# Performance work log

Measured on AMD Instinct MI355X. Metric: run time of the kernel, lower is better.

The kernel has to match this reference:

```python
import jax, jax.numpy as jnp
import numpy as np

N_HEADS = 16


def setup_inputs() -> dict:
    key = jax.random.key(0)
    ks = jax.random.split(key, 5)
    B, S, D = 2, 2048, 1024
    scale = 1.0 / np.sqrt(D)
    return {
        "x": jax.random.normal(ks[0], (B, S, D), dtype=jnp.float32),
        "w_in": jax.random.normal(ks[1], (3 * D, D), dtype=jnp.float32) * scale,
        "b_in": jax.random.normal(ks[2], (3 * D,), dtype=jnp.float32) * 0.01,
        "w_out": jax.random.normal(ks[3], (D, D), dtype=jnp.float32) * scale,
        "b_out": jax.random.normal(ks[4], (D,), dtype=jnp.float32) * 0.01,
        "mask": 1,
    }


def reference(x, w_in, b_in, w_out, b_out, mask):
    b, s, d = x.shape
    h = N_HEADS
    dh = d // h
    # fused QKV projection (torch Linear: x @ W^T + b)
    qkv = jnp.einsum("bsd,ed->bse", x, w_in) + b_in  # [b, s, 3d]
    q, k, v = jnp.split(qkv, 3, axis=-1)
    # [b, s, d] -> [b, h, s, dh]
    q = q.reshape(b, s, h, dh).transpose(0, 2, 1, 3)
    k = k.reshape(b, s, h, dh).transpose(0, 2, 1, 3)
    v = v.reshape(b, s, h, dh).transpose(0, 2, 1, 3)
    att = jnp.einsum("bhqd,bhkd->bhqk", q, k)
    if mask:
        causal = jnp.triu(jnp.ones((s, s), dtype=bool), k=1)
        att = jnp.where(causal, -jnp.inf, att)
    att = att / jnp.sqrt(jnp.asarray(dh, att.dtype))
    att = jax.nn.softmax(att, axis=-1)
    out = jnp.einsum("bhqk,bhkd->bhqd", att, v)  # [b, h, s, dh]
    out = out.transpose(0, 2, 1, 3).reshape(b, s, d)
    return jnp.einsum("bsd,ed->bse", out, w_out) + b_out
```

## Files before the change

kernel.cpp:

```cpp
#include <hip/hip_runtime.h>
#include <hip/hip_bf16.h>
#include <cmath>

typedef __hip_bfloat16 bf16;
typedef short v8s __attribute__((ext_vector_type(8)));
typedef short v4s __attribute__((ext_vector_type(4)));
typedef float v4f __attribute__((ext_vector_type(4)));

#define AS1(p) ((__attribute__((address_space(1))) void*)(p))
#define AS3(p) ((__attribute__((address_space(3))) void*)(p))

__device__ __forceinline__ v4f mfma_bf16(v8s a, v8s b, v4f c) {
    return __builtin_amdgcn_mfma_f32_16x16x32_bf16(a, b, c, 0, 0, 0);
}

__device__ __forceinline__ short bf16_bits(float f) {
    return __builtin_bit_cast(short, __float2bfloat16(f));
}

__global__ __launch_bounds__(256)
void cvt_all(const float* __restrict__ x, const float* __restrict__ w_in,
             const float* __restrict__ w_out, bf16* __restrict__ xb,
             bf16* __restrict__ wib, bf16* __restrict__ wob)
{
    const int i = blockIdx.x * 256 + threadIdx.x;
    const float* src; bf16* dst; int j;
    if (i < 1048576)      { src = x;     dst = xb;  j = i; }
    else if (i < 1835008) { src = w_in;  dst = wib; j = i - 1048576; }
    else                  { src = w_out; dst = wob; j = i - 1835008; }
    const float4 v = ((const float4*)src)[j];
    v4s p;
    p.x = bf16_bits(v.x); p.y = bf16_bits(v.y);
    p.z = bf16_bits(v.z); p.w = bf16_bits(v.w);
    ((v4s*)dst)[j] = p;
}

template<int NF>
__global__ __launch_bounds__(256)
void gemm_bt(const bf16* __restrict__ A, const bf16* __restrict__ Bt,
             const float* __restrict__ bias, bf16* __restrict__ C,
             float* __restrict__ Cf, int N, int K, int lda)
{
    constexpr int BN = NF * 32;
    __shared__ __align__(16) bf16 As[128 * 64];
    __shared__ __align__(16) bf16 Bs[BN * 64];

    const int t    = threadIdx.x;
    const int lane = t & 63;
    const int wave = t >> 6;
    const int l16  = lane & 15;
    const int quad = lane >> 4;
    const int m0   = blockIdx.y * 128;
    const int n0   = blockIdx.x * BN;
    const int wm   = (wave >> 1) * 64;
    const int wn   = (wave & 1) * (NF * 16);

    const v4f zf = {0.f, 0.f, 0.f, 0.f};
    v4f acc[4][NF];
#pragma unroll
    for (int i = 0; i < 4; ++i)
#pragma unroll
        for (int j = 0; j < NF; ++j) acc[i][j] = zf;

    const int sr  = t >> 3;
    const int swz = ((t & 7) ^ (sr & 7)) * 8;
    const bf16* gA = A  + (size_t)(m0 + sr) * lda + swz;
    const bf16* gB = Bt + (size_t)(n0 + sr) * K + swz;
    char* lA = (char*)As + t * 16;
    char* lB = (char*)Bs + t * 16;

    for (int k0 = 0; k0 < K; k0 += 64) {
#pragma unroll
        for (int i = 0; i < 4; ++i)
            __builtin_amdgcn_global_load_lds(AS1(gA + (size_t)(i * 32) * lda + k0),
                                             AS3(lA + i * 4096), 16, 0, 0);
#pragma unroll
        for (int i = 0; i < NF; ++i)
            __builtin_amdgcn_global_load_lds(AS1(gB + (size_t)(i * 32) * K + k0),
                                             AS3(lB + i * 4096), 16, 0, 0);
        __syncthreads();

        v8s af[4][2], bfr[NF][2];
#pragma unroll
        for (int mi = 0; mi < 4; ++mi)
#pragma unroll
            for (int ks = 0; ks < 2; ++ks)
                af[mi][ks] = *(const v8s*)(As + (wm + mi * 16 + l16) * 64
                                           + (((ks * 4 + quad) ^ (l16 & 7)) * 8));
#pragma unroll
        for (int ni = 0; ni < NF; ++ni)
#pragma unroll
            for (int ks = 0; ks < 2; ++ks)
                bfr[ni][ks] = *(const v8s*)(Bs + (wn + ni * 16 + l16) * 64
                                            + (((ks * 4 + quad) ^ (l16 & 7)) * 8));
#pragma unroll
        for (int ks = 0; ks < 2; ++ks)
#pragma unroll
            for (int mi = 0; mi < 4; ++mi)
#pragma unroll
                for (int ni = 0; ni < NF; ++ni)
                    acc[mi][ni] = mfma_bf16(af[mi][ks], bfr[ni][ks], acc[mi][ni]);
        __syncthreads();
    }

#pragma unroll
    for (int ni = 0; ni < NF; ++ni) {
        const int col = n0 + wn + ni * 16 + l16;
        const float bv = bias[col];
#pragma unroll
        for (int mi = 0; mi < 4; ++mi) {
#pragma unroll
            for (int r = 0; r < 4; ++r) {
                const int row = m0 + wm + mi * 16 + quad * 4 + r;
                const float fv = acc[mi][ni][r] + bv;
                if (Cf) Cf[(size_t)row * N + col] = fv;
                else    C [(size_t)row * N + col] = __float2bfloat16(fv);
            }
        }
    }
}

__global__ __launch_bounds__(256)
void vtrans(const bf16* __restrict__ qkv, bf16* __restrict__ Vt)
{
    __shared__ short Ts[64][72];
    const int t  = threadIdx.x;
    const int st = blockIdx.x;
    const int bh = blockIdx.y;
    const int b = bh >> 4, h = bh & 15;
    const int s0 = st * 64;
    {
        const int i = t >> 2, j0 = (t & 3) * 16;
        const bf16* src = qkv + (size_t)(b * 2048 + s0 + i) * 3072 + 2048 + h * 64 + j0;
        const v8s a0 = *(const v8s*)(src);
        const v8s a1 = *(const v8s*)(src + 8);
        *(v8s*)&Ts[i][j0]     = a0;
        *(v8s*)&Ts[i][j0 + 8] = a1;
    }
    __syncthreads();
    {
        const int d = t >> 2, seg = (t & 3) * 16;
        v8s o0, o1;
#pragma unroll
        for (int m = 0; m < 8; ++m) { o0[m] = Ts[seg + m][d]; o1[m] = Ts[seg + 8 + m][d]; }
        bf16* dst = Vt + (size_t)(bh * 64 + d) * 2048 + s0 + seg;
        *(v8s*)dst       = o0;
        *(v8s*)(dst + 8) = o1;
    }
}

#define M_STATIC 14.0f
__global__ __launch_bounds__(256)
void attn(bf16* __restrict__ qkv, const bf16* __restrict__ Vt)
{
    __shared__ __align__(16) bf16 Ks[2][64 * 64];
    __shared__ __align__(16) bf16 Vs[2][64 * 64];
    __shared__ __align__(16) short Ps[4][16 * 72];

    const int t    = threadIdx.x;
    const int lane = t & 63;
    const int w    = t >> 6;
    const int l16  = lane & 15;
    const int quad = lane >> 4;
    const int id   = blockIdx.x;
    const int bh   = id & 31;
    const int qb   = 31 - (id >> 5);
    const int b = bh >> 4, h = bh & 15;
    const int T = qb + 1;
    const int rowq = qb * 64 + w * 16;

    v8s qf[2];
    {
        const bf16* Qb = qkv + (size_t)(b * 2048 + rowq + l16) * 3072 + h * 64 + quad * 8;
        qf[0] = *(const v8s*)(Qb);
        qf[1] = *(const v8s*)(Qb + 32);
    }

    const int sr  = t >> 3;
    const int swz = ((t & 7) ^ (sr & 7)) * 8;
    const bf16* kbase = qkv + (size_t)(b * 2048 + sr) * 3072 + 1024 + h * 64 + swz;
    const bf16* vbase = Vt + (size_t)(bh * 64 + sr) * 2048 + swz;
    char* kd = (char*)&Ks[0][0] + t * 16;
    char* vd = (char*)&Vs[0][0] + t * 16;

    __builtin_amdgcn_global_load_lds(AS1(kbase),                     AS3(kd),        16, 0, 0);
    __builtin_amdgcn_global_load_lds(AS1(kbase + (size_t)32 * 3072), AS3(kd + 4096), 16, 0, 0);
    __builtin_amdgcn_global_load_lds(AS1(vbase),                     AS3(vd),        16, 0, 0);
    __builtin_amdgcn_global_load_lds(AS1(vbase + (size_t)32 * 2048), AS3(vd + 4096), 16, 0, 0);

    const v4f zf = {0.f, 0.f, 0.f, 0.f};
    v4f o[4] = {zf, zf, zf, zf};
    float lsum[4] = {0.f, 0.f, 0.f, 0.f};
    short* Pw = &Ps[w][0];
    const int xsw = (l16 & 7) * 8;

    for (int tile = 0; tile < T; ++tile) {
        const int buf = tile & 1;
        __syncthreads();
        if (tile + 1 < T) {
            const int nb = buf ^ 1;
            const bf16* ksrc = kbase + (size_t)((tile + 1) * 64) * 3072;
            const bf16* vsrc = vbase + (tile + 1) * 64;
            char* kdn = (char*)&Ks[nb][0] + t * 16;
            char* vdn = (char*)&Vs[nb][0] + t * 16;
            __builtin_amdgcn_global_load_lds(AS1(ksrc),                     AS3(kdn),        16, 0, 0);
            __builtin_amdgcn_global_load_lds(AS1(ksrc + (size_t)32 * 3072), AS3(kdn + 4096), 16, 0, 0);
            __builtin_amdgcn_global_load_lds(AS1(vsrc),                     AS3(vdn),        16, 0, 0);
            __builtin_amdgcn_global_load_lds(AS1(vsrc + (size_t)32 * 2048), AS3(vdn + 4096), 16, 0, 0);
        }

        v4f s[4] = {zf, zf, zf, zf};
#pragma unroll
        for (int ks = 0; ks < 2; ++ks)
#pragma unroll
            for (int ct = 0; ct < 4; ++ct) {
                const v8s kf = *(const v8s*)(&Ks[buf][0] + (ct * 16 + l16) * 64
                                             + (((ks * 4 + quad) * 8) ^ xsw));
                s[ct] = mfma_bf16(qf[ks], kf, s[ct]);
            }

        if (tile == T - 1) {
            const int colb = tile * 64;
            const int rowb = rowq + quad * 4;
#pragma unroll
            for (int ct = 0; ct < 4; ++ct) {
                const int col = colb + ct * 16 + l16;
#pragma unroll
                for (int r = 0; r < 4; ++r) {
                    const float p = (col > rowb + r)
                        ? 0.f : __expf(fmaf(s[ct][r], 0.125f, -M_STATIC));
                    lsum[r] += p;
                    Pw[(quad * 4 + r) * 72 + ct * 16 + l16] = bf16_bits(p);
                }
            }
        } else {
#pragma unroll
            for (int ct = 0; ct < 4; ++ct)
#pragma unroll
                for (int r = 0; r < 4; ++r) {
                    const float p = __expf(fmaf(s[ct][r], 0.125f, -M_STATIC));
                    lsum[r] += p;
                    Pw[(quad * 4 + r) * 72 + ct * 16 + l16] = bf16_bits(p);
                }
        }
        asm volatile("s_waitcnt lgkmcnt(0)" ::: "memory");

#pragma unroll
        for (int ks = 0; ks < 2; ++ks) {
            const v8s pf = *(const v8s*)(Pw + l16 * 72 + ks * 32 + quad * 8);
#pragma unroll
            for (int nt = 0; nt < 4; ++nt) {
                const v8s vf = *(const v8s*)(&Vs[buf][0] + (nt * 16 + l16) * 64
                                             + (((ks * 4 + quad) * 8) ^ xsw));
                o[nt] = mfma_bf16(pf, vf, o[nt]);
            }
        }
    }

#pragma unroll
    for (int r = 0; r < 4; ++r) {
        float l = lsum[r];
        l += __shfl_xor(l, 1); l += __shfl_xor(l, 2);
        l += __shfl_xor(l, 4); l += __shfl_xor(l, 8);
        lsum[r] = fmaxf(l, 1e-30f);
    }

#pragma unroll
    for (int nt = 0; nt < 4; ++nt)
#pragma unroll
        for (int r = 0; r < 4; ++r) {
            const int row = rowq + quad * 4 + r;
            qkv[(size_t)(b * 2048 + row) * 3072 + 2048 + h * 64 + nt * 16 + l16] =
                __float2bfloat16(o[nt][r] / lsum[r]);
        }
}

extern "C" void kernel_launch(void* const* d_in, const int* in_sizes, int n_in,
                              void* d_out, int out_size, void* d_ws, size_t ws_size,
                              hipStream_t stream)
{
    (void)in_sizes; (void)n_in; (void)out_size; (void)ws_size;
    const float* x     = (const float*)d_in[0];
    const float* w_in  = (const float*)d_in[1];
    const float* b_in  = (const float*)d_in[2];
    const float* w_out = (const float*)d_in[3];
    const float* b_out = (const float*)d_in[4];
    float* out = (float*)d_out;

    bf16* ws     = (bf16*)d_ws;
    bf16* xb     = ws;
    bf16* w_inb  = xb     + (size_t)4096 * 1024;
    bf16* w_outb = w_inb  + (size_t)3072 * 1024;
    bf16* qkv    = w_outb + (size_t)1024 * 1024;
    bf16* vt     = (bf16*)d_out;

    cvt_all<<<8192, 256, 0, stream>>>(x, w_in, w_out, xb, w_inb, w_outb);

    gemm_bt<4><<<dim3(24, 32), dim3(256), 0, stream>>>(xb, w_inb, b_in, qkv, nullptr,
                                                       3072, 1024, 1024);
    vtrans<<<dim3(32, 32), dim3(256), 0, stream>>>(qkv, vt);
    attn<<<1024, 256, 0, stream>>>(qkv, vt);
    gemm_bt<2><<<dim3(16, 32), dim3(256), 0, stream>>>(qkv + 2048, w_outb, b_out, nullptr,
                                                       out, 1024, 1024, 3072);
}
```

Baseline: 194.2 us.

## Double-buffer GEMM LDS tiles with K-step 32 and prefetch next tile

Reworks the bf16 GEMM main loop to use two LDS buffers of half depth (K tile 32 instead of 64). The next tile's async global-to-LDS loads are issued right after the barrier so they overlap the current tile's MFMA work, and one of the two barriers per iteration is dropped. The swizzle is rewritten for the 32-wide rows. Each iteration now does half the MFMA work, so there is more barrier overhead per unit of compute. The B-tile staging also assumes NF is 2 or 4.

```diff
diff --git a/kernel.cpp b/kernel.cpp
--- a/kernel.cpp
+++ b/kernel.cpp
@@ -42,8 +42,8 @@
              float* __restrict__ Cf, int N, int K, int lda)
 {
     constexpr int BN = NF * 32;
-    __shared__ __align__(16) bf16 As[128 * 64];
-    __shared__ __align__(16) bf16 Bs[BN * 64];
+    __shared__ __align__(16) bf16 As[2][128 * 32];
+    __shared__ __align__(16) bf16 Bs[2][BN * 32];
 
     const int t    = threadIdx.x;
     const int lane = t & 63;
@@ -62,45 +62,44 @@
 #pragma unroll
         for (int j = 0; j < NF; ++j) acc[i][j] = zf;
 
-    const int sr  = t >> 3;
-    const int swz = ((t & 7) ^ (sr & 7)) * 8;
-    const bf16* gA = A  + (size_t)(m0 + sr) * lda + swz;
-    const bf16* gB = Bt + (size_t)(n0 + sr) * K + swz;
-    char* lA = (char*)As + t * 16;
-    char* lB = (char*)Bs + t * 16;
-
-    for (int k0 = 0; k0 < K; k0 += 64) {
-#pragma unroll
-        for (int i = 0; i < 4; ++i)
-            __builtin_amdgcn_global_load_lds(AS1(gA + (size_t)(i * 32) * lda + k0),
-                                             AS3(lA + i * 4096), 16, 0, 0);
-#pragma unroll
-        for (int i = 0; i < NF; ++i)
-            __builtin_amdgcn_global_load_lds(AS1(gB + (size_t)(i * 32) * K + k0),
-                                             AS3(lB + i * 4096), 16, 0, 0);
+    const int sr = t >> 2;
+    const int g  = ((t & 3) ^ ((sr >> 1) & 3)) * 8;
+    const bf16* gA = A  + (size_t)(m0 + sr) * lda + g;
+    const bf16* gB = Bt + (size_t)(n0 + sr) * K + g;
+
+    auto stage = [&](int kt, int buf) {
+        const int k0 = kt * 32;
+        char* lA = (char*)&As[buf][0] + t * 16;
+        char* lB = (char*)&Bs[buf][0] + t * 16;
+        __builtin_amdgcn_global_load_lds(AS1(gA + k0),                    AS3(lA),        16, 0, 0);
+        __builtin_amdgcn_global_load_lds(AS1(gA + (size_t)64 * lda + k0), AS3(lA + 4096), 16, 0, 0);
+        __builtin_amdgcn_global_load_lds(AS1(gB + k0),                    AS3(lB),        16, 0, 0);
+        if (NF == 4)
+            __builtin_amdgcn_global_load_lds(AS1(gB + (size_t)64 * K + k0), AS3(lB + 4096), 16, 0, 0);
+    };
+
+    stage(0, 0);
+    const int KT = K >> 5;
+    const int xs = ((l16 >> 1) & 3) * 8;
+    for (int kt = 0; kt < KT; ++kt) {
+        const int buf = kt & 1;
         __syncthreads();
-
-        v8s af[4][2], bfr[NF][2];
+        if (kt + 1 < KT) stage(kt + 1, buf ^ 1);
+
+        v8s af[4], bfr[NF];
 #pragma unroll
         for (int mi = 0; mi < 4; ++mi)
-#pragma unroll
-            for (int ks = 0; ks < 2; ++ks)
-                af[mi][ks] = *(const v8s*)(As + (wm + mi * 16 + l16) * 64
-                                           + (((ks * 4 + quad) ^ (l16 & 7)) * 8));
+            af[mi] = *(const v8s*)(&As[buf][0] + (wm + mi * 16 + l16) * 32
+                                   + ((quad * 8) ^ xs));
 #pragma unroll
         for (int ni = 0; ni < NF; ++ni)
-#pragma unroll
-            for (int ks = 0; ks < 2; ++ks)
-                bfr[ni][ks] = *(const v8s*)(Bs + (wn + ni * 16 + l16) * 64
-                                            + (((ks * 4 + quad) ^ (l16 & 7)) * 8));
-#pragma unroll
-        for (int ks = 0; ks < 2; ++ks)
-#pragma unroll
-            for (int mi = 0; mi < 4; ++mi)
-#pragma unroll
-                for (int ni = 0; ni < NF; ++ni)
-                    acc[mi][ni] = mfma_bf16(af[mi][ks], bfr[ni][ks], acc[mi][ni]);
-        __syncthreads();
+            bfr[ni] = *(const v8s*)(&Bs[buf][0] + (wn + ni * 16 + l16) * 32
+                                    + ((quad * 8) ^ xs));
+#pragma unroll
+        for (int mi = 0; mi < 4; ++mi)
+#pragma unroll
+            for (int ni = 0; ni < NF; ++ni)
+                acc[mi][ni] = mfma_bf16(af[mi], bfr[ni], acc[mi][ni]);
     }
 
 #pragma unroll
```

Result: faster. 188.2 us (-3.1%).
